# Performance work log

Hardware: AMD Instinct MI355X
Metric: run time of the kernel (lower is better)

Reference implementation:

```python
import jax, jax.numpy as jnp
import numpy as np

N = 100000   # nodes
E = 400000   # edges
G = 64       # graphs in batch
D_IN = 20
D_H = 1024   # 4 * 256
D_FC = 128


def _w(key, shape, fan_in):
    return jax.random.normal(key, shape, jnp.float32) / np.sqrt(fan_in).astype(np.float32)


def setup_inputs() -> dict:
    key = jax.random.key(0)
    ks = jax.random.split(key, 14)
    x = jax.random.normal(ks[0], (N, D_IN), jnp.float32)
    edge_index = jax.random.randint(ks[1], (2, E), 0, N)
    batch = jnp.sort(jax.random.randint(ks[2], (N,), 0, G))
    return {
        "x": x,
        "edge_index": edge_index,
        "batch": batch,
        # SAGEConv 1: lin_l (neighbors, with bias), lin_r (root, no bias)
        "W1l": _w(ks[3], (D_H, D_IN), D_IN),
        "b1l": _w(ks[4], (D_H,), D_IN),
        "W1r": _w(ks[5], (D_H, D_IN), D_IN),
        # SAGEConv 2
        "W2l": _w(ks[6], (D_H, D_H), D_H),
        "b2l": _w(ks[7], (D_H,), D_H),
        "W2r": _w(ks[8], (D_H, D_H), D_H),
        # MLP head
        "Wf1": _w(ks[9], (D_FC, D_H), D_H),
        "bf1": _w(ks[10], (D_FC,), D_H),
        "Wf2": _w(ks[11], (1, D_FC), D_FC),
        "bf2": _w(ks[12], (1,), D_FC),
    }


def _sage_mean(h, src, dst, inv_deg, Wl, bl, Wr):
    # mean over incoming neighbors (src -> dst), then lin_l(agg) + lin_r(h)
    agg = jax.ops.segment_sum(h[src], dst, num_segments=N) * inv_deg  # [N, d]
    return agg @ Wl.T + bl + h @ Wr.T


def reference(x, edge_index, batch, W1l, b1l, W1r, W2l, b2l, W2r, Wf1, bf1, Wf2, bf2):
    src, dst = edge_index[0], edge_index[1]
    deg = jax.ops.segment_sum(jnp.ones((E,), jnp.float32), dst, num_segments=N)
    inv_deg = (1.0 / jnp.maximum(deg, 1.0))[:, None]  # nodes w/o in-edges -> 0 agg

    h = jnp.tanh(_sage_mean(x, src, dst, inv_deg, W1l, b1l, W1r))
    h = jnp.tanh(_sage_mean(h, src, dst, inv_deg, W2l, b2l, W2r))
    g = jax.ops.segment_sum(h, batch, num_segments=G)            # global_add_pool [G, D_H]
    y = jax.nn.leaky_relu(g @ Wf1.T + bf1, negative_slope=0.2)
    return y @ Wf2.T + bf2                                        # [G, 1]
```

## Files before the change

kernel.cpp:

```cpp
#include <hip/hip_runtime.h>
#include <stdint.h>
#include <stddef.h>

#define N_NODES 100000
#define N_EDGES 400000
#define NG      64
#define DIN     20
#define DH      1024
#define DFC     128
#define M_PAD   100096
#define MTILES  782
#define NBLK    391
#define CHUNK_T 128

typedef __attribute__((ext_vector_type(8))) short bf16x8_t;
typedef __attribute__((ext_vector_type(4))) float f32x4_t;

__device__ __forceinline__ float bf2f(uint32_t u){
  union { uint32_t i; float f; } v; v.i = u << 16; return v.f;
}
__device__ __forceinline__ uint32_t pk_bf16(float lo, float hi){
  uint32_t r;
  asm("v_cvt_pk_bf16_f32 %0, %1, %2" : "=v"(r) : "v"(lo), "v"(hi));
  return r;
}
__device__ __forceinline__ float tanhf_fast(float x){
  float t = __expf(2.0f * x);
  return 1.0f - 2.0f * __builtin_amdgcn_rcpf(1.0f + t);
}
__device__ __forceinline__ void gll16(const void* g, void* l){
  __builtin_amdgcn_global_load_lds(
      (const __attribute__((address_space(1))) unsigned int*)g,
      (__attribute__((address_space(3))) unsigned int*)l, 16, 0, 0);
}
__device__ __forceinline__ int xcd_swz(int bid, int nwg){
  if (nwg & 7) return bid;
  return (bid & 7) * (nwg >> 3) + (bid >> 3);
}
#define BARRIER() asm volatile("s_barrier" ::: "memory")

__global__ void k_diag(float* __restrict__ out, float v){
  out[threadIdx.x] = v;
}

__global__ void k_deg(const int* __restrict__ dstn, int* __restrict__ deg){
  int e = blockIdx.x * 256 + threadIdx.x;
  if (e < N_EDGES) atomicAdd(&deg[dstn[e]], 1);
}

__global__ void k_scan1(const int* __restrict__ deg, int* __restrict__ rowoff,
                        int* __restrict__ part){
  __shared__ int sb[256];
  const int t = threadIdx.x;
  const int n = blockIdx.x * 256 + t;
  int v = (n < N_NODES) ? deg[n] : 0;
  sb[t] = v;
  __syncthreads();
  for (int off = 1; off < 256; off <<= 1){
    int u = (t >= off) ? sb[t - off] : 0;
    __syncthreads();
    sb[t] += u;
    __syncthreads();
  }
  int incl = sb[t];
  if (n < N_NODES) rowoff[n] = incl - v;
  if (t == 255) part[blockIdx.x] = incl;
}

__global__ void k_scan2(int* part, int nblk){
  __shared__ int sb[512];
  const int t = threadIdx.x;
  int v = (t < nblk) ? part[t] : 0;
  sb[t] = v;
  __syncthreads();
  for (int off = 1; off < 512; off <<= 1){
    int u = (t >= off) ? sb[t - off] : 0;
    __syncthreads();
    sb[t] += u;
    __syncthreads();
  }
  if (t < nblk) part[t] = sb[t] - v;
}

__global__ void k_scan3(int* __restrict__ rowoff, const int* __restrict__ part){
  int n = blockIdx.x * 256 + threadIdx.x;
  if (n < N_NODES) rowoff[n] += part[blockIdx.x];
  if (n == 0) rowoff[N_NODES] = N_EDGES;
}

__global__ void k_fill(const int* __restrict__ src, const int* __restrict__ dstn,
                       const int* __restrict__ rowoff, int* __restrict__ cursor,
                       int* __restrict__ colx){
  int e = blockIdx.x * 256 + threadIdx.x;
  if (e < N_EDGES){
    int d = dstn[e];
    int p = rowoff[d] + atomicAdd(&cursor[d], 1);
    colx[p] = src[e];
  }
}

__global__ void k_pack(const float* __restrict__ x, const int* __restrict__ rowoff,
                       const int* __restrict__ colx, uint16_t* __restrict__ Ap){
  const int n = blockIdx.x * 256 + threadIdx.x;
  if (n >= M_PAD) return;
  uint4 o[8];
  if (n < N_NODES){
    f32x4_t a0 = {}, a1 = {}, a2 = {}, a3 = {}, a4 = {};
    const int e0 = rowoff[n], e1 = rowoff[n + 1];
    for (int e = e0; e < e1; e++){
      const f32x4_t* xr = (const f32x4_t*)(x + (size_t)colx[e] * DIN);
      a0 += xr[0]; a1 += xr[1]; a2 += xr[2]; a3 += xr[3]; a4 += xr[4];
    }
    const float inv = (e1 > e0) ? 1.f / (float)(e1 - e0) : 0.f;
    a0 *= inv; a1 *= inv; a2 *= inv; a3 *= inv; a4 *= inv;
    const f32x4_t* xs = (const f32x4_t*)(x + (size_t)n * DIN);
    f32x4_t b0 = xs[0], b1 = xs[1], b2 = xs[2], b3 = xs[3], b4 = xs[4];
    o[0] = make_uint4(pk_bf16(a0[0],a0[1]), pk_bf16(a0[2],a0[3]), pk_bf16(a1[0],a1[1]), pk_bf16(a1[2],a1[3]));
    o[1] = make_uint4(pk_bf16(a2[0],a2[1]), pk_bf16(a2[2],a2[3]), pk_bf16(a3[0],a3[1]), pk_bf16(a3[2],a3[3]));
    o[2] = make_uint4(pk_bf16(a4[0],a4[1]), pk_bf16(a4[2],a4[3]), pk_bf16(b0[0],b0[1]), pk_bf16(b0[2],b0[3]));
    o[3] = make_uint4(pk_bf16(b1[0],b1[1]), pk_bf16(b1[2],b1[3]), pk_bf16(b2[0],b2[1]), pk_bf16(b2[2],b2[3]));
    o[4] = make_uint4(pk_bf16(b3[0],b3[1]), pk_bf16(b3[2],b3[3]), pk_bf16(b4[0],b4[1]), pk_bf16(b4[2],b4[3]));
    o[5] = make_uint4(0,0,0,0); o[6] = o[5]; o[7] = o[5];
  } else {
    o[0] = make_uint4(0,0,0,0);
    for (int i = 1; i < 8; i++) o[i] = o[0];
  }
  uint4* dst = (uint4*)(Ap + (size_t)n * 64);
#pragma unroll
  for (int i = 0; i < 8; i++) dst[i] = o[i];
}

__global__ void k_prep(const float* __restrict__ W1l, const float* __restrict__ W1r,
                       uint16_t* __restrict__ Bp,
                       const float* __restrict__ W2l, const float* __restrict__ W2r,
                       uint16_t* __restrict__ B2){
  const int b = blockIdx.x;
  if (b < 4){
    const int j = b * 256 + threadIdx.x;
    if (j >= DH) return;
    const f32x4_t* wl = (const f32x4_t*)(W1l + (size_t)j * DIN);
    const f32x4_t* wr = (const f32x4_t*)(W1r + (size_t)j * DIN);
    f32x4_t a0 = wl[0], a1 = wl[1], a2 = wl[2], a3 = wl[3], a4 = wl[4];
    f32x4_t b0 = wr[0], b1 = wr[1], b2 = wr[2], b3 = wr[3], b4 = wr[4];
    uint4 o[8];
    o[0] = make_uint4(pk_bf16(a0[0],a0[1]), pk_bf16(a0[2],a0[3]), pk_bf16(a1[0],a1[1]), pk_bf16(a1[2],a1[3]));
    o[1] = make_uint4(pk_bf16(a2[0],a2[1]), pk_bf16(a2[2],a2[3]), pk_bf16(a3[0],a3[1]), pk_bf16(a3[2],a3[3]));
    o[2] = make_uint4(pk_bf16(a4[0],a4[1]), pk_bf16(a4[2],a4[3]), pk_bf16(b0[0],b0[1]), pk_bf16(b0[2],b0[3]));
    o[3] = make_uint4(pk_bf16(b1[0],b1[1]), pk_bf16(b1[2],b1[3]), pk_bf16(b2[0],b2[1]), pk_bf16(b2[2],b2[3]));
    o[4] = make_uint4(pk_bf16(b3[0],b3[1]), pk_bf16(b3[2],b3[3]), pk_bf16(b4[0],b4[1]), pk_bf16(b4[2],b4[3]));
    o[5] = make_uint4(0,0,0,0); o[6] = o[5]; o[7] = o[5];
    uint4* dst = (uint4*)(Bp + (size_t)j * 64);
#pragma unroll
    for (int i = 0; i < 8; i++) dst[i] = o[i];
    return;
  }
  int q = (b - 4) * 256 + threadIdx.x;
  const int sel = q >= 262144;
  if (sel) q -= 262144;
  const int j = q >> 8;
  const int k4 = (q & 255) * 4;
  const float* w = sel ? W2r : W2l;
  float4 f = *(const float4*)(w + (size_t)j * 1024 + k4);
  uint2 o;
  o.x = pk_bf16(f.x, f.y);
  o.y = pk_bf16(f.z, f.w);
  *(uint2*)(B2 + (size_t)j * 2048 + sel * 1024 + k4) = o;
}

__global__ __launch_bounds__(256) void k_l1g(
    const uint16_t* __restrict__ Ap, const uint16_t* __restrict__ Bp,
    const float* __restrict__ bias, uint16_t* __restrict__ h1)
{
  __shared__ uint16_t lds[16384];
  const int wg = xcd_swz(blockIdx.x, gridDim.x);
  const int mt = wg >> 3, jt = wg & 7;
  const int tid = threadIdx.x;
  const int lane = tid & 63, w = tid >> 6;
  const int wm = w >> 1, wn = w & 1;
  char* ldsb = (char*)lds;

  const int rgrp = lane >> 3;
  const int sl   = lane & 7;
  const int sw   = sl ^ rgrp;
#pragma unroll
  for (int t = 0; t < 4; t++){
    const int r0 = w * 32 + t * 8;
    gll16((const char*)Ap + (size_t)(mt * 128 + r0 + rgrp) * 128 + sw * 16,
          ldsb + r0 * 128);
    gll16((const char*)Bp + (size_t)(jt * 128 + r0 + rgrp) * 128 + sw * 16,
          ldsb + 16384 + r0 * 128);
  }
  __syncthreads();

  f32x4_t acc[4][4] = {};
  const int ks = lane >> 4;
  const int rA = wm * 64 + (lane & 15);
  const int rB = wn * 64 + (lane & 15);
#pragma unroll
  for (int kt = 0; kt < 2; kt++){
    bf16x8_t af[4], bg[4];
#pragma unroll
    for (int mi = 0; mi < 4; mi++){
      int r = rA + mi * 16;
      af[mi] = *(const bf16x8_t*)(ldsb + r * 128 + (((kt * 4 + ks) ^ (r & 7)) << 4));
    }
#pragma unroll
    for (int ni = 0; ni < 4; ni++){
      int r = rB + ni * 16;
      bg[ni] = *(const bf16x8_t*)(ldsb + 16384 + r * 128 + (((kt * 4 + ks) ^ (r & 7)) << 4));
    }
#pragma unroll
    for (int mi = 0; mi < 4; mi++)
#pragma unroll
      for (int ni = 0; ni < 4; ni++)
        acc[mi][ni] = __builtin_amdgcn_mfma_f32_16x16x32_bf16(bg[ni], af[mi], acc[mi][ni], 0, 0, 0);
  }

  __syncthreads();
  const int c4 = (lane >> 4) * 4;
#pragma unroll
  for (int ni = 0; ni < 4; ni++){
    const int colL = wn * 64 + ni * 16 + c4;
    const f32x4_t bs = *(const f32x4_t*)(bias + jt * 128 + colL);
    const int b16 = colL >> 3;
    const int hh  = (colL >> 2) & 1;
#pragma unroll
    for (int mi = 0; mi < 4; mi++){
      const int r = wm * 64 + mi * 16 + (lane & 15);
      uint2 o;
      o.x = pk_bf16(tanhf_fast(acc[mi][ni][0] + bs[0]), tanhf_fast(acc[mi][ni][1] + bs[1]));
      o.y = pk_bf16(tanhf_fast(acc[mi][ni][2] + bs[2]), tanhf_fast(acc[mi][ni][3] + bs[3]));
      *(uint2*)(ldsb + r * 256 + ((b16 ^ (r & 15)) << 4) + hh * 8) = o;
    }
  }
  __syncthreads();
  char* dst0 = (char*)(h1 + (size_t)(mt * 128) * DH + jt * 128);
#pragma unroll
  for (int k = 0; k < 8; k++){
    const int c = tid + k * 256;
    const int r = c >> 4, b16 = c & 15;
    uint4 v = *(const uint4*)(ldsb + r * 256 + ((b16 ^ (r & 15)) << 4));
    *(uint4*)(dst0 + (size_t)r * DH * 2 + b16 * 16) = v;
  }
}

__global__ void k_agg2(const uint16_t* __restrict__ h1, const int* __restrict__ rowoff,
                       const int* __restrict__ colx, uint16_t* __restrict__ aggc,
                       int row0){
  const int half = threadIdx.x >> 7;
  const int t = threadIdx.x & 127;
  const int nl = blockIdx.x * 2 + half;
  const int n = row0 + nl;
  uint4* out = (uint4*)aggc;
  const size_t ro = (size_t)nl * 128 + t;
  if (n >= N_NODES){ out[ro] = make_uint4(0u,0u,0u,0u); return; }
  const int e0 = rowoff[n], e1 = rowoff[n + 1];
  float f0=0.f,f1=0.f,f2=0.f,f3=0.f,f4=0.f,f5=0.f,f6=0.f,f7=0.f;
  const uint4* H = (const uint4*)h1;
  for (int e = e0; e < e1; e++){
    uint4 u = H[(size_t)colx[e] * 128 + t];
    f0 += bf2f(u.x); f1 += bf2f(u.x >> 16);
    f2 += bf2f(u.y); f3 += bf2f(u.y >> 16);
    f4 += bf2f(u.z); f5 += bf2f(u.z >> 16);
    f6 += bf2f(u.w); f7 += bf2f(u.w >> 16);
  }
  const float inv = (e1 > e0) ? 1.f / (float)(e1 - e0) : 0.f;
  uint4 o;
  o.x = pk_bf16(f0 * inv, f1 * inv);
  o.y = pk_bf16(f2 * inv, f3 * inv);
  o.z = pk_bf16(f4 * inv, f5 * inv);
  o.w = pk_bf16(f6 * inv, f7 * inv);
  out[ro] = o;
}

__global__ __launch_bounds__(512) void k_gemm(
    const uint16_t* __restrict__ A0, const uint16_t* __restrict__ A1,
    const uint16_t* __restrict__ B2, const float* __restrict__ bias,
    const int* __restrict__ batch, float* __restrict__ gbuf, int row0)
{
  __shared__ char ldsb[131072];
  const int wg = xcd_swz(blockIdx.x, gridDim.x);
  const int mt = wg >> 2, jtg = wg & 3;
  const int tid = threadIdx.x;
  const int lane = tid & 63, w = tid >> 6;
  const int wm = w >> 2, wn = w & 3;

  const int aw_row = w * 8 + (lane >> 3);
  const size_t slotb = (size_t)(((lane & 7) ^ (lane >> 3)) << 4);

  auto stageA = [&](int half, int t2){
    const char* gb = (t2 < 16) ? (const char*)A0 : (const char*)A1;
    const size_t ktc = (size_t)(t2 & 15) * 128;
    char* lb = ldsb + (t2 & 1) * 65536 + half * 16384 + w * 1024;
    const size_t r0 = (size_t)(mt * 256 + half * 128 + aw_row);
    gll16(gb + r0 * 2048 + ktc + slotb, lb);
    gll16(gb + (r0 + 64) * 2048 + ktc + slotb, lb + 8192);
  };
  auto stageB = [&](int half, int t2){
    const size_t ktc = (size_t)t2 * 128;
    char* lb = ldsb + (t2 & 1) * 65536 + 32768 + half * 16384 + w * 1024;
    const size_t r0 = (size_t)(jtg * 256 + half * 128 + aw_row);
    gll16((const char*)B2 + r0 * 4096 + ktc + slotb, lb);
    gll16((const char*)B2 + (r0 + 64) * 4096 + ktc + slotb, lb + 8192);
  };

  stageB(0, 0); stageB(1, 0); stageA(0, 0); stageA(1, 0);
  stageB(0, 1); stageB(1, 1); stageA(0, 1);
  asm volatile("s_waitcnt vmcnt(6)" ::: "memory");
  BARRIER();

  f32x4_t acc[8][4] = {};
  const int ks = lane >> 4;
  const int rA = wm * 128 + (lane & 15);
  const int rB = wn * 64 + (lane & 15);

  for (int kt = 0; kt < 32; ++kt){
    const char* lA = ldsb + (kt & 1) * 65536;
    const char* lB = lA + 32768;
    bf16x8_t bg[4][2], af03[4][2], af47[4][2];
#pragma unroll
    for (int n = 0; n < 4; n++){
      int r = rB + n * 16;
      bg[n][0] = *(const bf16x8_t*)(lB + r * 128 + ((ks ^ (r & 7)) << 4));
      bg[n][1] = *(const bf16x8_t*)(lB + r * 128 + (((4 + ks) ^ (r & 7)) << 4));
    }
#pragma unroll
    for (int m = 0; m < 4; m++){
      int r = rA + m * 16;
      af03[m][0] = *(const bf16x8_t*)(lA + r * 128 + ((ks ^ (r & 7)) << 4));
      af03[m][1] = *(const bf16x8_t*)(lA + r * 128 + (((4 + ks) ^ (r & 7)) << 4));
    }
    asm volatile("s_waitcnt lgkmcnt(0)" ::: "memory");
    __builtin_amdgcn_sched_barrier(0);
    BARRIER();
    if (kt < 31) stageA(1, kt + 1);
    if (kt < 30){ stageB(0, kt + 2); stageB(1, kt + 2); stageA(0, kt + 2); }
#pragma unroll
    for (int m = 0; m < 4; m++){
      int r = rA + 64 + m * 16;
      af47[m][0] = *(const bf16x8_t*)(lA + r * 128 + ((ks ^ (r & 7)) << 4));
      af47[m][1] = *(const bf16x8_t*)(lA + r * 128 + (((4 + ks) ^ (r & 7)) << 4));
    }
    __builtin_amdgcn_s_setprio(1);
#pragma unroll
    for (int m = 0; m < 4; m++)
#pragma unroll
      for (int n = 0; n < 4; n++)
        acc[m][n] = __builtin_amdgcn_mfma_f32_16x16x32_bf16(af03[m][0], bg[n][0], acc[m][n], 0, 0, 0);
#pragma unroll
    for (int m = 0; m < 4; m++)
#pragma unroll
      for (int n = 0; n < 4; n++)
        acc[m][n] = __builtin_amdgcn_mfma_f32_16x16x32_bf16(af03[m][1], bg[n][1], acc[m][n], 0, 0, 0);
#pragma unroll
    for (int m = 0; m < 4; m++)
#pragma unroll
      for (int n = 0; n < 4; n++)
        acc[4 + m][n] = __builtin_amdgcn_mfma_f32_16x16x32_bf16(af47[m][0], bg[n][0], acc[4 + m][n], 0, 0, 0);
#pragma unroll
    for (int m = 0; m < 4; m++)
#pragma unroll
      for (int n = 0; n < 4; n++)
        acc[4 + m][n] = __builtin_amdgcn_mfma_f32_16x16x32_bf16(af47[m][1], bg[n][1], acc[4 + m][n], 0, 0, 0);
    __builtin_amdgcn_s_setprio(0);
    if (kt < 30) asm volatile("s_waitcnt vmcnt(6)" ::: "memory");
    else         asm volatile("s_waitcnt vmcnt(0)" ::: "memory");
    BARRIER();
  }

  const int rowbase = row0 + mt * 256 + wm * 128;
  const int colbase = jtg * 256 + wn * 64;
  int bt[8][4];
#pragma unroll
  for (int mi = 0; mi < 8; mi++)
#pragma unroll
    for (int i = 0; i < 4; i++){
      int R = rowbase + mi * 16 + (lane >> 4) * 4 + i;
      bt[mi][i] = (R < N_NODES) ? batch[R] : -1;
    }
  const int c0 = rowbase       < N_NODES ? rowbase       : N_NODES - 1;
  const int c1 = rowbase + 127 < N_NODES ? rowbase + 127 : N_NODES - 1;
  const int gmin = batch[c0], gmax = batch[c1];

#pragma unroll
  for (int ni = 0; ni < 4; ni++){
    const int col = colbase + ni * 16 + (lane & 15);
    const float bs = bias[col];
    float v[8][4];
#pragma unroll
    for (int mi = 0; mi < 8; mi++)
#pragma unroll
      for (int i = 0; i < 4; i++)
        v[mi][i] = tanhf_fast(acc[mi][ni][i] + bs);
    for (int g = gmin; g <= gmax; g++){
      float s_ = 0.f;
#pragma unroll
      for (int mi = 0; mi < 8; mi++)
#pragma unroll
        for (int i = 0; i < 4; i++)
          s_ += (bt[mi][i] == g) ? v[mi][i] : 0.f;
      s_ += __shfl_xor(s_, 16);
      s_ += __shfl_xor(s_, 32);
      if (lane < 16) atomicAdd(&gbuf[g * DH + col], s_);
    }
  }
}

__global__ void k_head(const float* __restrict__ gbuf, const float* __restrict__ Wf1,
                       const float* __restrict__ bf1, const float* __restrict__ Wf2,
                       const float* __restrict__ bf2, float* __restrict__ out){
  const int gg = blockIdx.x, j = threadIdx.x;
  const float* grow = gbuf + (size_t)gg * DH;
  const float* wr = Wf1 + (size_t)j * DH;
  float acc = bf1[j];
  for (int k = 0; k < DH; k++) acc = fmaf(grow[k], wr[k], acc);
  float y = acc > 0.f ? acc : 0.2f * acc;
  __shared__ float sb[DFC];
  sb[j] = y * Wf2[j];
  __syncthreads();
  for (int off = 64; off > 0; off >>= 1){
    if (j < off) sb[j] += sb[j + off];
    __syncthreads();
  }
  if (j == 0) out[gg] = sb[0] + bf2[0];
}

extern "C" void kernel_launch(void* const* d_in, const int* in_sizes, int n_in,
                              void* d_out, int out_size, void* d_ws, size_t ws_size,
                              hipStream_t stream){
  const float* x   = (const float*)d_in[0];
  const int*   ei  = (const int*)d_in[1];
  const int*   src = ei;
  const int*   dst = ei + N_EDGES;
  const int*   batch = (const int*)d_in[2];
  const float* W1l = (const float*)d_in[3];
  const float* b1l = (const float*)d_in[4];
  const float* W1r = (const float*)d_in[5];
  const float* W2l = (const float*)d_in[6];
  const float* b2l = (const float*)d_in[7];
  const float* W2r = (const float*)d_in[8];
  const float* Wf1 = (const float*)d_in[9];
  const float* bf1 = (const float*)d_in[10];
  const float* Wf2 = (const float*)d_in[11];
  const float* bf2 = (const float*)d_in[12];
  float* out = (float*)d_out;
  (void)in_sizes; (void)n_in; (void)out_size;

  char* ws = (char*)d_ws;
  size_t off = 0;
  auto alloc = [&](size_t bytes) -> void* {
    void* p = (void*)(ws + off);
    off = (off + bytes + 255) & ~(size_t)255;
    return p;
  };
  uint16_t* h1   = (uint16_t*)alloc((size_t)M_PAD * DH * 2);
  uint16_t* Ap   = (uint16_t*)alloc((size_t)M_PAD * 64 * 2);
  uint16_t* Bp   = (uint16_t*)alloc((size_t)DH * 64 * 2);
  uint16_t* B2   = (uint16_t*)alloc((size_t)DH * 2048 * 2);
  int*      deg  = (int*)alloc((size_t)N_NODES * 4);
  int*      curs = (int*)alloc((size_t)N_NODES * 4);
  float*    gbuf = (float*)alloc((size_t)NG * DH * 4);
  int*      rowo = (int*)alloc((size_t)(N_NODES + 1) * 4);
  int*      colx = (int*)alloc((size_t)N_EDGES * 4);
  int*      part = (int*)alloc((size_t)NBLK * 4);
  long long remain = (long long)ws_size - (long long)off;
  int chunk_t = (int)(remain / (128LL * 2048LL));
  if (chunk_t > CHUNK_T) chunk_t = CHUNK_T;
  chunk_t &= ~1;
  if (chunk_t < 2){
    k_diag<<<1, 64, 0, stream>>>(out, (float)ws_size);
    return;
  }
  uint16_t* aggc = (uint16_t*)alloc((size_t)chunk_t * 128 * DH * 2);

  const size_t zset = (size_t)((char*)gbuf - (char*)deg) + (size_t)NG * DH * 4;
  hipMemsetAsync(deg, 0, zset, stream);

  k_deg  <<<(N_EDGES + 255) / 256, 256, 0, stream>>>(dst, deg);
  k_scan1<<<NBLK, 256, 0, stream>>>(deg, rowo, part);
  k_scan2<<<1, 512, 0, stream>>>(part, NBLK);
  k_scan3<<<NBLK, 256, 0, stream>>>(rowo, part);
  k_fill <<<(N_EDGES + 255) / 256, 256, 0, stream>>>(src, dst, rowo, curs, colx);
  k_pack <<<NBLK, 256, 0, stream>>>(x, rowo, colx, Ap);
  k_prep <<<4 + 2048, 256, 0, stream>>>(W1l, W1r, Bp, W2l, W2r, B2);
  k_l1g  <<<MTILES * 8, 256, 0, stream>>>(Ap, Bp, b1l, h1);

  for (int t0 = 0; t0 < MTILES; ){
    int ct = MTILES - t0 < chunk_t ? MTILES - t0 : chunk_t;
    int row0 = t0 * 128;
    k_agg2<<<ct * 64, 256, 0, stream>>>(h1, rowo, colx, aggc, row0);
    k_gemm<<<(ct / 2) * 4, 512, 0, stream>>>(aggc, h1 + (size_t)row0 * DH,
                                             B2, b2l, batch, gbuf, row0);
    t0 += ct;
  }
  k_head <<<NG, DFC, 0, stream>>>(gbuf, Wf1, bf1, Wf2, bf2, out);
}
```

Measured before the change: 775.0 us.

## Load GEMM B operand directly from global into registers, stage only A in LDS

The main GEMM no longer stages the weight (B) tiles through LDS. Each wave now loads its B fragments straight from global memory into registers, one k-step ahead. Only A is double-buffered in LDS, which halves the LDS footprint and could allow higher occupancy. The hand-tuned vmcnt/barrier pipeline with a two-stage lookahead is replaced by plain __syncthreads, so there is less latency hiding and more redundant global B traffic across the wm waves, relying on L2 hits.

```diff
diff --git a/kernel.cpp b/kernel.cpp
--- a/kernel.cpp
+++ b/kernel.cpp
@@ -37,7 +37,6 @@
   if (nwg & 7) return bid;
   return (bid & 7) * (nwg >> 3) + (bid >> 3);
 }
-#define BARRIER() asm volatile("s_barrier" ::: "memory")
 
 __global__ void k_diag(float* __restrict__ out, float v){
   out[threadIdx.x] = v;
@@ -278,7 +277,7 @@
     const uint16_t* __restrict__ B2, const float* __restrict__ bias,
     const int* __restrict__ batch, float* __restrict__ gbuf, int row0)
 {
-  __shared__ char ldsb[131072];
+  __shared__ char ldsb[65536];
   const int wg = xcd_swz(blockIdx.x, gridDim.x);
   const int mt = wg >> 2, jtg = wg & 3;
   const int tid = threadIdx.x;
@@ -288,84 +287,64 @@
   const int aw_row = w * 8 + (lane >> 3);
   const size_t slotb = (size_t)(((lane & 7) ^ (lane >> 3)) << 4);
 
-  auto stageA = [&](int half, int t2){
+  auto stageA = [&](int t2){
     const char* gb = (t2 < 16) ? (const char*)A0 : (const char*)A1;
     const size_t ktc = (size_t)(t2 & 15) * 128;
-    char* lb = ldsb + (t2 & 1) * 65536 + half * 16384 + w * 1024;
-    const size_t r0 = (size_t)(mt * 256 + half * 128 + aw_row);
+    char* lb = ldsb + (t2 & 1) * 32768 + w * 1024;
+    const size_t r0 = (size_t)(mt * 256 + aw_row);
     gll16(gb + r0 * 2048 + ktc + slotb, lb);
     gll16(gb + (r0 + 64) * 2048 + ktc + slotb, lb + 8192);
+    gll16(gb + (r0 + 128) * 2048 + ktc + slotb, lb + 16384);
+    gll16(gb + (r0 + 192) * 2048 + ktc + slotb, lb + 24576);
   };
-  auto stageB = [&](int half, int t2){
-    const size_t ktc = (size_t)t2 * 128;
-    char* lb = ldsb + (t2 & 1) * 65536 + 32768 + half * 16384 + w * 1024;
-    const size_t r0 = (size_t)(jtg * 256 + half * 128 + aw_row);
-    gll16((const char*)B2 + r0 * 4096 + ktc + slotb, lb);
-    gll16((const char*)B2 + (r0 + 64) * 4096 + ktc + slotb, lb + 8192);
-  };
-
-  stageB(0, 0); stageB(1, 0); stageA(0, 0); stageA(1, 0);
-  stageB(0, 1); stageB(1, 1); stageA(0, 1);
-  asm volatile("s_waitcnt vmcnt(6)" ::: "memory");
-  BARRIER();
+
+  const int ks = lane >> 4;
+  const char* Bg = (const char*)B2
+                 + (size_t)(jtg * 256 + wn * 64 + (lane & 15)) * 4096 + ((size_t)ks << 4);
+
+  bf16x8_t bg[8], bgN[8];
+  stageA(0);
+#pragma unroll
+  for (int n = 0; n < 4; n++)
+#pragma unroll
+    for (int q = 0; q < 2; q++)
+      bg[n * 2 + q] = *(const bf16x8_t*)(Bg + (size_t)n * 65536 + q * 64);
+  stageA(1);
+  __syncthreads();
 
   f32x4_t acc[8][4] = {};
-  const int ks = lane >> 4;
   const int rA = wm * 128 + (lane & 15);
-  const int rB = wn * 64 + (lane & 15);
 
   for (int kt = 0; kt < 32; ++kt){
-    const char* lA = ldsb + (kt & 1) * 65536;
-    const char* lB = lA + 32768;
-    bf16x8_t bg[4][2], af03[4][2], af47[4][2];
-#pragma unroll
-    for (int n = 0; n < 4; n++){
-      int r = rB + n * 16;
-      bg[n][0] = *(const bf16x8_t*)(lB + r * 128 + ((ks ^ (r & 7)) << 4));
-      bg[n][1] = *(const bf16x8_t*)(lB + r * 128 + (((4 + ks) ^ (r & 7)) << 4));
-    }
-#pragma unroll
-    for (int m = 0; m < 4; m++){
+    const char* lA = ldsb + (kt & 1) * 32768;
+    if (kt < 31){
+#pragma unroll
+      for (int n = 0; n < 4; n++)
+#pragma unroll
+        for (int q = 0; q < 2; q++)
+          bgN[n * 2 + q] = *(const bf16x8_t*)(Bg + (size_t)n * 65536
+                                              + (size_t)(kt + 1) * 128 + q * 64);
+    }
+    if (kt < 31) stageA(kt + 1);
+    bf16x8_t af[8][2];
+#pragma unroll
+    for (int m = 0; m < 8; m++){
       int r = rA + m * 16;
-      af03[m][0] = *(const bf16x8_t*)(lA + r * 128 + ((ks ^ (r & 7)) << 4));
-      af03[m][1] = *(const bf16x8_t*)(lA + r * 128 + (((4 + ks) ^ (r & 7)) << 4));
-    }
-    asm volatile("s_waitcnt lgkmcnt(0)" ::: "memory");
-    __builtin_amdgcn_sched_barrier(0);
-    BARRIER();
-    if (kt < 31) stageA(1, kt + 1);
-    if (kt < 30){ stageB(0, kt + 2); stageB(1, kt + 2); stageA(0, kt + 2); }
-#pragma unroll
-    for (int m = 0; m < 4; m++){
-      int r = rA + 64 + m * 16;
-      af47[m][0] = *(const bf16x8_t*)(lA + r * 128 + ((ks ^ (r & 7)) << 4));
-      af47[m][1] = *(const bf16x8_t*)(lA + r * 128 + (((4 + ks) ^ (r & 7)) << 4));
-    }
-    __builtin_amdgcn_s_setprio(1);
-#pragma unroll
-    for (int m = 0; m < 4; m++)
-#pragma unroll
-      for (int n = 0; n < 4; n++)
-        acc[m][n] = __builtin_amdgcn_mfma_f32_16x16x32_bf16(af03[m][0], bg[n][0], acc[m][n], 0, 0, 0);
-#pragma unroll
-    for (int m = 0; m < 4; m++)
-#pragma unroll
-      for (int n = 0; n < 4; n++)
-        acc[m][n] = __builtin_amdgcn_mfma_f32_16x16x32_bf16(af03[m][1], bg[n][1], acc[m][n], 0, 0, 0);
-#pragma unroll
-    for (int m = 0; m < 4; m++)
-#pragma unroll
-      for (int n = 0; n < 4; n++)
-        acc[4 + m][n] = __builtin_amdgcn_mfma_f32_16x16x32_bf16(af47[m][0], bg[n][0], acc[4 + m][n], 0, 0, 0);
-#pragma unroll
-    for (int m = 0; m < 4; m++)
-#pragma unroll
-      for (int n = 0; n < 4; n++)
-        acc[4 + m][n] = __builtin_amdgcn_mfma_f32_16x16x32_bf16(af47[m][1], bg[n][1], acc[4 + m][n], 0, 0, 0);
-    __builtin_amdgcn_s_setprio(0);
-    if (kt < 30) asm volatile("s_waitcnt vmcnt(6)" ::: "memory");
-    else         asm volatile("s_waitcnt vmcnt(0)" ::: "memory");
-    BARRIER();
+      af[m][0] = *(const bf16x8_t*)(lA + r * 128 + ((ks ^ (r & 7)) << 4));
+      af[m][1] = *(const bf16x8_t*)(lA + r * 128 + (((4 + ks) ^ (r & 7)) << 4));
+    }
+#pragma unroll
+    for (int m = 0; m < 8; m++)
+#pragma unroll
+      for (int n = 0; n < 4; n++){
+        acc[m][n] = __builtin_amdgcn_mfma_f32_16x16x32_bf16(af[m][0], bg[n * 2 + 0], acc[m][n], 0, 0, 0);
+        acc[m][n] = __builtin_amdgcn_mfma_f32_16x16x32_bf16(af[m][1], bg[n * 2 + 1], acc[m][n], 0, 0, 0);
+      }
+    __syncthreads();
+    if (kt < 31){
+#pragma unroll
+      for (int i = 0; i < 8; i++) bg[i] = bgN[i];
+    }
   }
 
   const int rowbase = row0 + mt * 256 + wm * 128;
```

Result: slower. 992.6 us (+28.1%).
